# Performance work log

Hardware: AMD Instinct MI355X
Metric: run time of the kernel (lower is better)

The kernel has to match this reference:

```python
import jax, jax.numpy as jnp
import numpy as np

MARGIN = 0.3
EPS = 1e-12  # guards sqrt at zero distance (diagonal)


def setup_inputs() -> dict:
    key = jax.random.key(0)
    k1, k2 = jax.random.split(key)
    features = jax.random.normal(k1, (8192, 256), dtype=jnp.float32)
    labels = jax.random.randint(k2, (8192,), 0, 512, dtype=jnp.int64)
    return {"features": features, "labels": labels}


def reference(features, labels):
    # L2 normalize rows (F.normalize default: p=2, dim=1, eps=1e-12)
    norm = jnp.linalg.norm(features, axis=1, keepdims=True)
    f = features / jnp.maximum(norm, 1e-12)

    # pairwise euclidean distances: ||a||^2 + ||b||^2 - 2 a.b, then sqrt
    sq = jnp.sum(f * f, axis=1)  # [N]
    gram = f @ f.T               # [N, N]
    d2 = sq[:, None] + sq[None, :] - 2.0 * gram
    dist = jnp.sqrt(jnp.clip(d2, EPS))  # [N, N]

    mask_pos = labels[:, None] == labels[None, :]  # includes diagonal, as in torch code

    hardest_pos = jnp.max(dist * mask_pos.astype(dist.dtype), axis=1)
    dist_neg = jnp.where(mask_pos, jnp.inf, dist)
    hardest_neg = jnp.min(dist_neg, axis=1)

    loss = jax.nn.relu(hardest_pos - hardest_neg + MARGIN)
    return jnp.mean(loss)
```

## Files before the change

### kernel.cpp

```cpp
#include <hip/hip_runtime.h>
#include <hip/hip_bf16.h>
#include <math.h>

#define N 8192
#define D 256
#define MARGIN 0.3f
#define EPS 1e-12f

#define BT 128
#define NJB (N / BT)
#define TOTAL_TRI (NJB * (NJB + 1) / 2)

typedef __attribute__((ext_vector_type(8))) short short8;
typedef __attribute__((ext_vector_type(4))) float floatx4;

static __device__ inline ushort f2bf(float f) {
    __hip_bfloat16 h = __float2bfloat16(f);
    return *reinterpret_cast<ushort*>(&h);
}


__global__ __launch_bounds__(256) void normalize_kernel(const float* __restrict__ x,
                                                        ushort* __restrict__ fn16t,
                                                        float* __restrict__ out) {
    __shared__ ushort lnorm[16][256];
    const int g    = blockIdx.x;
    const int t    = threadIdx.x;
    const int w    = t >> 6;
    const int lane = t & 63;
    if (g == 0 && t == 0) out[0] = 0.0f;

    #pragma unroll
    for (int rr = 0; rr < 4; rr++) {
        const int rl  = w * 4 + rr;
        const int row = g * 16 + rl;
        float4 v = ((const float4*)(x + (size_t)row * D))[lane];
        float s = v.x * v.x + v.y * v.y + v.z * v.z + v.w * v.w;
        #pragma unroll
        for (int off = 32; off; off >>= 1) s += __shfl_down(s, off);
        s = __shfl(s, 0);
        const float inv = 1.0f / fmaxf(sqrtf(s), 1e-12f);
        ushort4 b;
        b.x = f2bf(v.x * inv); b.y = f2bf(v.y * inv);
        b.z = f2bf(v.z * inv); b.w = f2bf(v.w * inv);
        *(ushort4*)(&lnorm[rl][lane * 4]) = b;
    }
    __syncthreads();
    const int kk = t >> 5;
    const int pp = (t & 31) * 2;
    ushort* base = fn16t + ((size_t)g * 8 + kk) * 512;
    #pragma unroll
    for (int e = 0; e < 2; e++) {
        const int p    = pp + e;
        const int quad = p >> 4;
        const int l15  = p & 15;
        *(short8*)(base + p * 8) = *(const short8*)(&lnorm[l15][kk * 32 + quad * 8]);
    }
}

__global__ __launch_bounds__(256, 3) void gram_kernel(const ushort* __restrict__ fn16t,
                                                      const int* __restrict__ lab,
                                                      float* __restrict__ gp_part,
                                                      float* __restrict__ gn_part) {
    __shared__ float rT[4][BT][17];
    __shared__ float cGp[BT][2], cGn[BT][2];

    const int bidx = blockIdx.x;
    const int idx  = (bidx & 7) * 260 + (bidx >> 3);
    const float c = 2.0f * NJB + 1.0f;
    int ib = (int)((c - sqrtf(c * c - 8.0f * (float)idx)) * 0.5f);
    while (ib > 0 && idx < ib * NJB - ib * (ib - 1) / 2) ib--;
    while (idx >= (ib + 1) * NJB - (ib + 1) * ib / 2) ib++;
    const int jb = ib + (idx - (ib * NJB - ib * (ib - 1) / 2));
    const bool offdiag = (jb > ib);
    const int i0 = ib * BT, j0 = jb * BT;

    const int t    = threadIdx.x;
    const int w    = t >> 6;
    const int lane = t & 63;
    const int wi   = w >> 1, wj = w & 1;
    const int quad = lane >> 4;
    const int l15  = lane & 15;

    const ushort* pA[4];
    const ushort* pB[4];
    #pragma unroll
    for (int m = 0; m < 4; m++)
        pA[m] = fn16t + ((size_t)(ib * 8 + wi * 4 + m)) * 4096 + lane * 8;
    #pragma unroll
    for (int n = 0; n < 4; n++)
        pB[n] = fn16t + ((size_t)(jb * 8 + wj * 4 + n)) * 4096 + lane * 8;

    floatx4 acc[4][4];
    #pragma unroll
    for (int m = 0; m < 4; m++)
        #pragma unroll
        for (int n = 0; n < 4; n++)
            acc[m][n] = (floatx4){0.f, 0.f, 0.f, 0.f};

    #pragma unroll
    for (int kk = 0; kk < 8; kk++) {
        short8 af[4], bf_[4];
        #pragma unroll
        for (int m = 0; m < 4; m++) af[m]  = *(const short8*)(pA[m] + kk * 512);
        #pragma unroll
        for (int n = 0; n < 4; n++) bf_[n] = *(const short8*)(pB[n] + kk * 512);
        #pragma unroll
        for (int m = 0; m < 4; m++)
            #pragma unroll
            for (int n = 0; n < 4; n++)
                acc[m][n] = __builtin_amdgcn_mfma_f32_16x16x32_bf16(af[m], bf_[n], acc[m][n], 0, 0, 0);
    }

    int labj[4];
    #pragma unroll
    for (int n = 0; n < 4; n++) labj[n] = lab[j0 + wj * 64 + n * 16 + l15];
    float gpc[4], gnc[4];
    #pragma unroll
    for (int n = 0; n < 4; n++) { gpc[n] = INFINITY; gnc[n] = -INFINITY; }

    #pragma unroll
    for (int m = 0; m < 4; m++) {
        const int4 li4 = *(const int4*)(lab + i0 + wi * 64 + m * 16 + quad * 4);
        const int labi[4] = {li4.x, li4.y, li4.z, li4.w};
        #pragma unroll
        for (int r = 0; r < 4; r++) {
            float pr = INFINITY, nr = -INFINITY;
            #pragma unroll
            for (int n = 0; n < 4; n++) {
                const float g = acc[m][n][r];
                const bool same = (labi[r] == labj[n]);
                const float selp = same ? g : INFINITY;
                const float seln = same ? -INFINITY : g;
                pr = fminf(pr, selp);           nr = fmaxf(nr, seln);
                gpc[n] = fminf(gpc[n], selp);   gnc[n] = fmaxf(gnc[n], seln);
            }
            if (offdiag) {
                const int irow = wi * 64 + m * 16 + quad * 4 + r;
                rT[(wj << 1) + 0][irow][l15] = pr;
                rT[(wj << 1) + 1][irow][l15] = nr;
            }
        }
    }
    #pragma unroll
    for (int n = 0; n < 4; n++) {
        float p = gpc[n], q2 = gnc[n];
        p  = fminf(p,  __shfl_xor(p, 16));  p  = fminf(p,  __shfl_xor(p, 32));
        q2 = fmaxf(q2, __shfl_xor(q2, 16)); q2 = fmaxf(q2, __shfl_xor(q2, 32));
        if (quad == 0) {
            const int col = wj * 64 + n * 16 + l15;
            cGp[col][wi] = p; cGn[col][wi] = q2;
        }
    }
    __syncthreads();
    if (t < BT) {
        gp_part[(size_t)ib * N + j0 + t] = fminf(cGp[t][0], cGp[t][1]);
        gn_part[(size_t)ib * N + j0 + t] = fmaxf(cGn[t][0], cGn[t][1]);
    } else if (offdiag) {
        const int i = t - BT;
        float p = INFINITY, nn = -INFINITY;
        #pragma unroll
        for (int k = 0; k < 16; k++) {
            p  = fminf(p,  fminf(rT[0][i][k], rT[2][i][k]));
            nn = fmaxf(nn, fmaxf(rT[1][i][k], rT[3][i][k]));
        }
        gp_part[(size_t)jb * N + i0 + i] = p;
        gn_part[(size_t)jb * N + i0 + i] = nn;
    }
}

__global__ __launch_bounds__(256) void reduce_kernel(const float* __restrict__ gp_part,
                                                     const float* __restrict__ gn_part,
                                                     float* __restrict__ out) {
    __shared__ float redp[32][5], redn[32][5];
    const int t  = threadIdx.x;
    const int r  = blockIdx.x * 32 + (t & 31);
    const int sg = t >> 5;
    float gp = INFINITY, gn = -INFINITY;
    #pragma unroll
    for (int q = 0; q < 8; q++) {
        const int s = sg * 8 + q;
        gp = fminf(gp, gp_part[(size_t)s * N + r]);
        gn = fmaxf(gn, gn_part[(size_t)s * N + r]);
    }
    gp = fminf(gp, __shfl_xor(gp, 32));
    gn = fmaxf(gn, __shfl_xor(gn, 32));
    const int w = t >> 6;
    if ((t & 63) < 32) { redp[t & 31][w] = gp; redn[t & 31][w] = gn; }
    __syncthreads();
    if (t < 32) {
        const float p  = fminf(fminf(redp[t][0], redp[t][1]), fminf(redp[t][2], redp[t][3]));
        const float nn = fmaxf(fmaxf(redn[t][0], redn[t][1]), fmaxf(redn[t][2], redn[t][3]));
        const float dp = sqrtf(fmaxf(2.0f - 2.0f * p,  EPS));
        const float dn = sqrtf(fmaxf(2.0f - 2.0f * nn, EPS));
        const float l  = dp - dn + MARGIN;
        float sum = (l > 0.0f) ? l : 0.0f;
        #pragma unroll
        for (int off = 16; off; off >>= 1) sum += __shfl_down(sum, off);
        if (t == 0) atomicAdd(out, sum * (1.0f / (float)N));
    }
}

extern "C" void kernel_launch(void* const* d_in, const int* in_sizes, int n_in,
                              void* d_out, int out_size, void* d_ws, size_t ws_size,
                              hipStream_t stream) {
    const float* x   = (const float*)d_in[0];
    const int*   lab = (const int*)d_in[1];
    float* out = (float*)d_out;

    char* ws = (char*)d_ws;
    ushort* fn16t   = (ushort*)ws;
    float*  gp_part = (float*)(ws + (size_t)N * D * 2);
    float*  gn_part = gp_part + (size_t)NJB * N;

    normalize_kernel<<<N / 16, 256, 0, stream>>>(x, fn16t, out);
    gram_kernel<<<TOTAL_TRI, 256, 0, stream>>>(fn16t, lab, gp_part, gn_part);
    reduce_kernel<<<N / 32, 256, 0, stream>>>(gp_part, gn_part, out);
}
```

Measured before the change: 98.53 us.

## Stage gram operand tiles through double-buffered LDS with async global-to-LDS loads

The gram kernel now loads A and B operand chunks into a double-buffered shared-memory area using global_load_lds. Each wave fetches a quarter of the chunks and the next k-slice is prefetched while the current one is multiplied. This removes the duplicate global loads where two waves read the same A or B fragments, and overlaps memory latency with MFMA work. In exchange it adds two barriers per k step and 32KB of LDS in a union with the reduction scratch, which may lower occupancy below the requested 3 blocks per CU.

```diff
diff --git a/kernel.cpp b/kernel.cpp
--- a/kernel.cpp
+++ b/kernel.cpp
@@ -17,6 +17,14 @@
 static __device__ inline ushort f2bf(float f) {
     __hip_bfloat16 h = __float2bfloat16(f);
     return *reinterpret_cast<ushort*>(&h);
+}
+
+#define BARRIER() do { asm volatile("" ::: "memory"); __builtin_amdgcn_s_barrier(); asm volatile("" ::: "memory"); } while (0)
+#define WAITVM(n) asm volatile("s_waitcnt vmcnt(" #n ")" ::: "memory")
+
+static __device__ inline void gload_lds16(const ushort* g, ushort* l) {
+    __builtin_amdgcn_global_load_lds((const __attribute__((address_space(1))) void*)g,
+                                     (__attribute__((address_space(3))) void*)l, 16, 0, 0);
 }
 
 
@@ -62,7 +70,10 @@
                                                       const int* __restrict__ lab,
                                                       float* __restrict__ gp_part,
                                                       float* __restrict__ gn_part) {
-    __shared__ float rT[4][BT][17];
+    __shared__ union {
+        ushort sbuf[2][8192];
+        float  rT[4][BT][17];
+    } u;
     __shared__ float cGp[BT][2], cGn[BT][2];
 
     const int bidx = blockIdx.x;
@@ -82,14 +93,16 @@
     const int quad = lane >> 4;
     const int l15  = lane & 15;
 
-    const ushort* pA[4];
-    const ushort* pB[4];
-    #pragma unroll
-    for (int m = 0; m < 4; m++)
-        pA[m] = fn16t + ((size_t)(ib * 8 + wi * 4 + m)) * 4096 + lane * 8;
-    #pragma unroll
-    for (int n = 0; n < 4; n++)
-        pB[n] = fn16t + ((size_t)(jb * 8 + wj * 4 + n)) * 4096 + lane * 8;
+    const int s0 = w * 4;
+    const ushort* gsrc[4];
+    #pragma unroll
+    for (int cc = 0; cc < 4; cc++) {
+        const int s = s0 + cc;
+        const int gchunk = (s < 8) ? (ib * 8 + s) : (jb * 8 + (s - 8));
+        gsrc[cc] = fn16t + (size_t)gchunk * 4096 + lane * 8;
+    }
+    const int aslot = wi * 4;
+    const int bslot = 8 + wj * 4;
 
     floatx4 acc[4][4];
     #pragma unroll
@@ -99,17 +112,35 @@
             acc[m][n] = (floatx4){0.f, 0.f, 0.f, 0.f};
 
     #pragma unroll
+    for (int cc = 0; cc < 4; cc++)
+        gload_lds16(gsrc[cc], &u.sbuf[0][(s0 + cc) * 512]);
+
+    #pragma unroll
     for (int kk = 0; kk < 8; kk++) {
+        if (kk < 7) {
+            #pragma unroll
+            for (int cc = 0; cc < 4; cc++)
+                gload_lds16(gsrc[cc] + (kk + 1) * 512, &u.sbuf[(kk + 1) & 1][(s0 + cc) * 512]);
+            WAITVM(4);
+        } else {
+            WAITVM(0);
+        }
+        BARRIER();
+
         short8 af[4], bf_[4];
         #pragma unroll
-        for (int m = 0; m < 4; m++) af[m]  = *(const short8*)(pA[m] + kk * 512);
-        #pragma unroll
-        for (int n = 0; n < 4; n++) bf_[n] = *(const short8*)(pB[n] + kk * 512);
+        for (int m = 0; m < 4; m++)
+            af[m]  = *(const short8*)&u.sbuf[kk & 1][(aslot + m) * 512 + lane * 8];
+        #pragma unroll
+        for (int n = 0; n < 4; n++)
+            bf_[n] = *(const short8*)&u.sbuf[kk & 1][(bslot + n) * 512 + lane * 8];
         #pragma unroll
         for (int m = 0; m < 4; m++)
             #pragma unroll
             for (int n = 0; n < 4; n++)
                 acc[m][n] = __builtin_amdgcn_mfma_f32_16x16x32_bf16(af[m], bf_[n], acc[m][n], 0, 0, 0);
+
+        BARRIER();
     }
 
     int labj[4];
@@ -137,8 +168,8 @@
             }
             if (offdiag) {
                 const int irow = wi * 64 + m * 16 + quad * 4 + r;
-                rT[(wj << 1) + 0][irow][l15] = pr;
-                rT[(wj << 1) + 1][irow][l15] = nr;
+                u.rT[(wj << 1) + 0][irow][l15] = pr;
+                u.rT[(wj << 1) + 1][irow][l15] = nr;
             }
         }
     }
@@ -161,8 +192,8 @@
         float p = INFINITY, nn = -INFINITY;
         #pragma unroll
         for (int k = 0; k < 16; k++) {
-            p  = fminf(p,  fminf(rT[0][i][k], rT[2][i][k]));
-            nn = fmaxf(nn, fmaxf(rT[1][i][k], rT[3][i][k]));
+            p  = fminf(p,  fminf(u.rT[0][i][k], u.rT[2][i][k]));
+            nn = fmaxf(nn, fmaxf(u.rT[1][i][k], u.rT[3][i][k]));
         }
         gp_part[(size_t)jb * N + i0 + i] = p;
         gn_part[(size_t)jb * N + i0 + i] = nn;
```

Result: slower. 114.0 us (+15.7%).

## Make gram kernel persistent, staging A row-panel in LDS across tiles

Applied to the files above, without the earlier changes.

The gram kernel becomes persistent with 512 blocks, each walking a contiguous run of 4-5 triangular tiles per XCD. The A row-panel (128 rows x 256 bf16) is loaded into LDS with global_load_lds and reused while ib is unchanged, instead of being re-read from global for every tile. The row-side reduction now uses wavefront shuffles rather than a padded LDS transpose buffer. The cost is 64 KB of LDS and lower occupancy (launch bounds 2), serialized tiles per block with extra barriers, and a possible load imbalance between blocks doing 5 and 4 tiles.

```diff
diff --git a/kernel.cpp b/kernel.cpp
--- a/kernel.cpp
+++ b/kernel.cpp
@@ -17,6 +17,11 @@
 static __device__ inline ushort f2bf(float f) {
     __hip_bfloat16 h = __float2bfloat16(f);
     return *reinterpret_cast<ushort*>(&h);
+}
+
+static __device__ inline void gload_lds16(const ushort* g, ushort* l) {
+    __builtin_amdgcn_global_load_lds((const __attribute__((address_space(1))) void*)g,
+                                     (__attribute__((address_space(3))) void*)l, 16, 0, 0);
 }
 
 
@@ -58,22 +63,19 @@
     }
 }
 
-__global__ __launch_bounds__(256, 3) void gram_kernel(const ushort* __restrict__ fn16t,
+__global__ __launch_bounds__(256, 2) void gram_kernel(const ushort* __restrict__ fn16t,
                                                       const int* __restrict__ lab,
                                                       float* __restrict__ gp_part,
                                                       float* __restrict__ gn_part) {
-    __shared__ float rT[4][BT][17];
+    __shared__ ushort aLds[64 * 512];
+    __shared__ float rowP[BT][2], rowN[BT][2];
     __shared__ float cGp[BT][2], cGn[BT][2];
 
-    const int bidx = blockIdx.x;
-    const int idx  = (bidx & 7) * 260 + (bidx >> 3);
-    const float c = 2.0f * NJB + 1.0f;
-    int ib = (int)((c - sqrtf(c * c - 8.0f * (float)idx)) * 0.5f);
-    while (ib > 0 && idx < ib * NJB - ib * (ib - 1) / 2) ib--;
-    while (idx >= (ib + 1) * NJB - (ib + 1) * ib / 2) ib++;
-    const int jb = ib + (idx - (ib * NJB - ib * (ib - 1) / 2));
-    const bool offdiag = (jb > ib);
-    const int i0 = ib * BT, j0 = jb * BT;
+    const int b    = blockIdx.x;
+    const int xcd  = b & 7;
+    const int loc  = b >> 3;
+    const int start = (loc < 4) ? loc * 5 : 20 + (loc - 4) * 4;
+    const int count = (loc < 4) ? 5 : 4;
 
     const int t    = threadIdx.x;
     const int w    = t >> 6;
@@ -82,90 +84,115 @@
     const int quad = lane >> 4;
     const int l15  = lane & 15;
 
-    const ushort* pA[4];
-    const ushort* pB[4];
-    #pragma unroll
-    for (int m = 0; m < 4; m++)
-        pA[m] = fn16t + ((size_t)(ib * 8 + wi * 4 + m)) * 4096 + lane * 8;
-    #pragma unroll
-    for (int n = 0; n < 4; n++)
-        pB[n] = fn16t + ((size_t)(jb * 8 + wj * 4 + n)) * 4096 + lane * 8;
-
-    floatx4 acc[4][4];
-    #pragma unroll
-    for (int m = 0; m < 4; m++)
+    int idx0 = xcd * 260 + start;
+    const float c = 2.0f * NJB + 1.0f;
+    int ib = (int)((c - sqrtf(c * c - 8.0f * (float)idx0)) * 0.5f);
+    while (ib > 0 && idx0 < ib * NJB - ib * (ib - 1) / 2) ib--;
+    while (idx0 >= (ib + 1) * NJB - (ib + 1) * ib / 2) ib++;
+    int jb = ib + (idx0 - (ib * NJB - ib * (ib - 1) / 2));
+
+    int cur_ib = -1;
+
+    for (int ti = 0; ti < count; ti++) {
+        const bool offdiag = (jb > ib);
+        const int i0 = ib * BT, j0 = jb * BT;
+
+        if (ib != cur_ib) {
+            __syncthreads();
+            const ushort* asrc = fn16t + (size_t)ib * 32768 + w * 8192 + lane * 8;
+            ushort* adst = aLds + w * 8192;
+            #pragma unroll
+            for (int i2 = 0; i2 < 16; i2++)
+                gload_lds16(asrc + i2 * 512, adst + i2 * 512);
+            __syncthreads();
+            cur_ib = ib;
+        }
+
+        const ushort* pB[4];
         #pragma unroll
         for (int n = 0; n < 4; n++)
-            acc[m][n] = (floatx4){0.f, 0.f, 0.f, 0.f};
-
-    #pragma unroll
-    for (int kk = 0; kk < 8; kk++) {
-        short8 af[4], bf_[4];
-        #pragma unroll
-        for (int m = 0; m < 4; m++) af[m]  = *(const short8*)(pA[m] + kk * 512);
-        #pragma unroll
-        for (int n = 0; n < 4; n++) bf_[n] = *(const short8*)(pB[n] + kk * 512);
+            pB[n] = fn16t + ((size_t)(jb * 8 + wj * 4 + n)) * 4096 + lane * 8;
+
+        floatx4 acc[4][4];
         #pragma unroll
         for (int m = 0; m < 4; m++)
             #pragma unroll
             for (int n = 0; n < 4; n++)
-                acc[m][n] = __builtin_amdgcn_mfma_f32_16x16x32_bf16(af[m], bf_[n], acc[m][n], 0, 0, 0);
-    }
-
-    int labj[4];
-    #pragma unroll
-    for (int n = 0; n < 4; n++) labj[n] = lab[j0 + wj * 64 + n * 16 + l15];
-    float gpc[4], gnc[4];
-    #pragma unroll
-    for (int n = 0; n < 4; n++) { gpc[n] = INFINITY; gnc[n] = -INFINITY; }
-
-    #pragma unroll
-    for (int m = 0; m < 4; m++) {
-        const int4 li4 = *(const int4*)(lab + i0 + wi * 64 + m * 16 + quad * 4);
-        const int labi[4] = {li4.x, li4.y, li4.z, li4.w};
-        #pragma unroll
-        for (int r = 0; r < 4; r++) {
-            float pr = INFINITY, nr = -INFINITY;
-            #pragma unroll
-            for (int n = 0; n < 4; n++) {
-                const float g = acc[m][n][r];
-                const bool same = (labi[r] == labj[n]);
-                const float selp = same ? g : INFINITY;
-                const float seln = same ? -INFINITY : g;
-                pr = fminf(pr, selp);           nr = fmaxf(nr, seln);
-                gpc[n] = fminf(gpc[n], selp);   gnc[n] = fmaxf(gnc[n], seln);
+                acc[m][n] = (floatx4){0.f, 0.f, 0.f, 0.f};
+
+        #pragma unroll
+        for (int kk = 0; kk < 8; kk++) {
+            short8 af[4], bf_[4];
+            #pragma unroll
+            for (int m = 0; m < 4; m++)
+                af[m] = *(const short8*)&aLds[((wi * 4 + m) * 8 + kk) * 512 + lane * 8];
+            #pragma unroll
+            for (int n = 0; n < 4; n++) bf_[n] = *(const short8*)(pB[n] + kk * 512);
+            #pragma unroll
+            for (int m = 0; m < 4; m++)
+                #pragma unroll
+                for (int n = 0; n < 4; n++)
+                    acc[m][n] = __builtin_amdgcn_mfma_f32_16x16x32_bf16(af[m], bf_[n], acc[m][n], 0, 0, 0);
+        }
+
+        int labj[4];
+        #pragma unroll
+        for (int n = 0; n < 4; n++) labj[n] = lab[j0 + wj * 64 + n * 16 + l15];
+        float gpc[4], gnc[4];
+        #pragma unroll
+        for (int n = 0; n < 4; n++) { gpc[n] = INFINITY; gnc[n] = -INFINITY; }
+
+        #pragma unroll
+        for (int m = 0; m < 4; m++) {
+            const int4 li4 = *(const int4*)(lab + i0 + wi * 64 + m * 16 + quad * 4);
+            const int labi[4] = {li4.x, li4.y, li4.z, li4.w};
+            #pragma unroll
+            for (int r = 0; r < 4; r++) {
+                float pr = INFINITY, nr = -INFINITY;
+                #pragma unroll
+                for (int n = 0; n < 4; n++) {
+                    const float g = acc[m][n][r];
+                    const bool same = (labi[r] == labj[n]);
+                    const float selp = same ? g : INFINITY;
+                    const float seln = same ? -INFINITY : g;
+                    pr = fminf(pr, selp);           nr = fmaxf(nr, seln);
+                    gpc[n] = fminf(gpc[n], selp);   gnc[n] = fmaxf(gnc[n], seln);
+                }
+                if (offdiag) {
+                    pr = fminf(pr, __shfl_xor(pr, 1));  pr = fminf(pr, __shfl_xor(pr, 2));
+                    pr = fminf(pr, __shfl_xor(pr, 4));  pr = fminf(pr, __shfl_xor(pr, 8));
+                    nr = fmaxf(nr, __shfl_xor(nr, 1));  nr = fmaxf(nr, __shfl_xor(nr, 2));
+                    nr = fmaxf(nr, __shfl_xor(nr, 4));  nr = fmaxf(nr, __shfl_xor(nr, 8));
+                    if (l15 == 0) {
+                        const int irow = wi * 64 + m * 16 + quad * 4 + r;
+                        rowP[irow][wj] = pr; rowN[irow][wj] = nr;
+                    }
+                }
             }
-            if (offdiag) {
-                const int irow = wi * 64 + m * 16 + quad * 4 + r;
-                rT[(wj << 1) + 0][irow][l15] = pr;
-                rT[(wj << 1) + 1][irow][l15] = nr;
+        }
+        #pragma unroll
+        for (int n = 0; n < 4; n++) {
+            float p = gpc[n], q2 = gnc[n];
+            p  = fminf(p,  __shfl_xor(p, 16));  p  = fminf(p,  __shfl_xor(p, 32));
+            q2 = fmaxf(q2, __shfl_xor(q2, 16)); q2 = fmaxf(q2, __shfl_xor(q2, 32));
+            if (quad == 0) {
+                const int col = wj * 64 + n * 16 + l15;
+                cGp[col][wi] = p; cGn[col][wi] = q2;
             }
         }
-    }
-    #pragma unroll
-    for (int n = 0; n < 4; n++) {
-        float p = gpc[n], q2 = gnc[n];
-        p  = fminf(p,  __shfl_xor(p, 16));  p  = fminf(p,  __shfl_xor(p, 32));
-        q2 = fmaxf(q2, __shfl_xor(q2, 16)); q2 = fmaxf(q2, __shfl_xor(q2, 32));
-        if (quad == 0) {
-            const int col = wj * 64 + n * 16 + l15;
-            cGp[col][wi] = p; cGn[col][wi] = q2;
-        }
-    }
-    __syncthreads();
-    if (t < BT) {
-        gp_part[(size_t)ib * N + j0 + t] = fminf(cGp[t][0], cGp[t][1]);
-        gn_part[(size_t)ib * N + j0 + t] = fmaxf(cGn[t][0], cGn[t][1]);
-    } else if (offdiag) {
-        const int i = t - BT;
-        float p = INFINITY, nn = -INFINITY;
-        #pragma unroll
-        for (int k = 0; k < 16; k++) {
-            p  = fminf(p,  fminf(rT[0][i][k], rT[2][i][k]));
-            nn = fmaxf(nn, fmaxf(rT[1][i][k], rT[3][i][k]));
-        }
-        gp_part[(size_t)jb * N + i0 + i] = p;
-        gn_part[(size_t)jb * N + i0 + i] = nn;
+        __syncthreads();
+        if (t < BT) {
+            gp_part[(size_t)ib * N + j0 + t] = fminf(cGp[t][0], cGp[t][1]);
+            gn_part[(size_t)ib * N + j0 + t] = fmaxf(cGn[t][0], cGn[t][1]);
+        } else if (offdiag) {
+            const int i = t - BT;
+            gp_part[(size_t)jb * N + i0 + i] = fminf(rowP[i][0], rowP[i][1]);
+            gn_part[(size_t)jb * N + i0 + i] = fmaxf(rowN[i][0], rowN[i][1]);
+        }
+        __syncthreads();
+
+        jb++;
+        if (jb == NJB) { ib++; jb = ib; }
     }
 }
 
@@ -214,6 +241,6 @@
     float*  gn_part = gp_part + (size_t)NJB * N;
 
     normalize_kernel<<<N / 16, 256, 0, stream>>>(x, fn16t, out);
-    gram_kernel<<<TOTAL_TRI, 256, 0, stream>>>(fn16t, lab, gp_part, gn_part);
+    gram_kernel<<<512, 256, 0, stream>>>(fn16t, lab, gp_part, gn_part);
     reduce_kernel<<<N / 32, 256, 0, stream>>>(gp_part, gn_part, out);
 }
```

After: 107.2 us. 8.8% more time.
